# Kernel optimization log

Hardware: AMD Instinct MI355X
Metric: run time of the kernel (lower is better)

The kernel has to match this reference:

```python
import jax, jax.numpy as jnp
import numpy as np

B, N, IN_DIM = 8, 2048, 256
H, D = 8, 64  # num_heads, output_dim (head dim)


def setup_inputs() -> dict:
    key = jax.random.key(0)
    ks = jax.random.split(key, 8)
    s_in = 1.0 / np.sqrt(IN_DIM)
    s_hd = 1.0 / np.sqrt(H * D)
    return {
        "msg": jax.random.normal(ks[0], (B, N, IN_DIM), dtype=jnp.float32),
        "Wq": jax.random.uniform(ks[1], (IN_DIM, H * D), jnp.float32, -s_in, s_in),
        "bq": jax.random.uniform(ks[2], (H * D,), jnp.float32, -s_in, s_in),
        "Wk": jax.random.uniform(ks[3], (IN_DIM, H * D), jnp.float32, -s_in, s_in),
        "bk": jax.random.uniform(ks[4], (H * D,), jnp.float32, -s_in, s_in),
        "Wv": jax.random.uniform(ks[5], (IN_DIM, H * D), jnp.float32, -s_in, s_in),
        "bv": jax.random.uniform(ks[6], (H * D,), jnp.float32, -s_in, s_in),
        "Wo": jax.random.uniform(ks[7], (H * D, D), jnp.float32, -s_hd, s_hd),
    }


def reference(msg, Wq, bq, Wk, bk, Wv, bv, Wo):
    b, n, _ = msg.shape
    # project and split heads: [B, H, N, D]
    q = (msg @ Wq + bq).reshape(b, n, H, D).transpose(0, 2, 1, 3)
    k = (msg @ Wk + bk).reshape(b, n, H, D).transpose(0, 2, 1, 3)
    v = (msg @ Wv + bv).reshape(b, n, H, D).transpose(0, 2, 1, 3)
    # scores in fp32 (original forces float under autocast(enabled=False))
    scores = jnp.einsum("bhnd,bhmd->bhnm", q.astype(jnp.float32), k.astype(jnp.float32)) / jnp.sqrt(jnp.float32(D))
    # exclude-self mask: zero diagonal -> masked with -1e9
    diag = jnp.eye(n, dtype=bool)  # [N, N]
    scores = jnp.where(diag, jnp.float32(-1e9), scores)
    attn = jax.nn.softmax(scores, axis=-1)
    ctx = jnp.einsum("bhnm,bhmd->bhnd", attn, v.astype(jnp.float32))
    ctx = ctx.transpose(0, 2, 1, 3).reshape(b, n, H * D)  # [B, N, H*D]
    return ctx @ Wo  # [B, N, D]
```

## Files before the change

### kernel.cpp

```cpp
#include <hip/hip_runtime.h>

typedef __bf16 bf16;
typedef __bf16 bf16x4 __attribute__((ext_vector_type(4)));
typedef __bf16 bf16x8 __attribute__((ext_vector_type(8)));
typedef float f32x4 __attribute__((ext_vector_type(4)));

#define SCLOG 0.1803368801111244f

constexpr int Bsz = 8, N = 2048, IN = 256, H = 8, D = 64;
constexpr int M = Bsz * N;
constexpr int HD = H * D;
constexpr int QKV = 3 * HD;

__global__ void cvt_msg(const float* __restrict__ in, bf16* __restrict__ out) {
    int i = blockIdx.x * blockDim.x + threadIdx.x;
    float4 v = ((const float4*)in)[i];
    bf16x4 o = { (bf16)v.x, (bf16)v.y, (bf16)v.z, (bf16)v.w };
    ((bf16x4*)out)[i] = o;
}

__global__ __launch_bounds__(256) void pack_w(
    const float* __restrict__ Wq, const float* __restrict__ Wk,
    const float* __restrict__ Wv, const float* __restrict__ bq,
    const float* __restrict__ bk, const float* __restrict__ bv,
    const float* __restrict__ Wo,
    bf16* __restrict__ Wt, float* __restrict__ bias, bf16* __restrict__ Wot) {
    __shared__ float Tt[32][33];
    const int tid = blockIdx.x;
    const int tx = threadIdx.x & 31, ty = threadIdx.x >> 5;
    if (tid < 384) {
        int wsel = tid >> 7, t = tid & 127;
        int k0 = (t >> 4) * 32, cl0 = (t & 15) * 32;
        const float* W = wsel == 0 ? Wq : (wsel == 1 ? Wk : Wv);
#pragma unroll
        for (int i = 0; i < 4; ++i)
            Tt[ty + i * 8][tx] = W[(size_t)(k0 + ty + i * 8) * HD + cl0 + tx];
        __syncthreads();
#pragma unroll
        for (int i = 0; i < 4; ++i)
            Wt[(size_t)(wsel * HD + cl0 + ty + i * 8) * IN + k0 + tx] =
                (bf16)Tt[tx][ty + i * 8];
    } else if (tid < 416) {
        int t = tid - 384;
        int r0 = (t >> 1) * 32, c0 = (t & 1) * 32;
#pragma unroll
        for (int i = 0; i < 4; ++i)
            Tt[ty + i * 8][tx] = Wo[(size_t)(r0 + ty + i * 8) * D + c0 + tx];
        __syncthreads();
#pragma unroll
        for (int i = 0; i < 4; ++i)
            Wot[(size_t)(c0 + ty + i * 8) * HD + r0 + tx] = (bf16)Tt[tx][ty + i * 8];
    } else {
        for (int v = threadIdx.x; v < QKV; v += 256)
            bias[v] = v < HD ? bq[v] : (v < 2 * HD ? bk[v - HD] : bv[v - 2 * HD]);
    }
}

__global__ __launch_bounds__(256) void qkv_gemm(
    const bf16* __restrict__ A, const bf16* __restrict__ Wt,
    const float* __restrict__ bias,
    bf16* __restrict__ Q, bf16* __restrict__ K, bf16* __restrict__ Vt) {
    __shared__ bf16 Tv[128][136];
    const int w = threadIdx.x >> 6, lane = threadIdx.x & 63;
    const int lr = lane & 15, lg = lane >> 4;
    const int mblk = blockIdx.x * 128;
    const int m0 = mblk + w * 32;
    const int c0 = blockIdx.y * 128;

    f32x4 acc[2][8] = {};
    const bf16* ap0 = A + (size_t)(m0 + lr) * IN + lg * 8;
    const bf16* ap1 = A + (size_t)(m0 + 16 + lr) * IN + lg * 8;
    const bf16* bp  = Wt + (size_t)(c0 + lr) * IN + lg * 8;

#pragma unroll
    for (int ks = 0; ks < 8; ++ks) {
        bf16x8 a0 = *(const bf16x8*)(ap0 + ks * 32);
        bf16x8 a1 = *(const bf16x8*)(ap1 + ks * 32);
#pragma unroll
        for (int nt = 0; nt < 8; ++nt) {
            bf16x8 bf = *(const bf16x8*)(bp + (size_t)nt * 16 * IN + ks * 32);
            acc[0][nt] = __builtin_amdgcn_mfma_f32_16x16x32_bf16(a0, bf, acc[0][nt], 0, 0, 0);
            acc[1][nt] = __builtin_amdgcn_mfma_f32_16x16x32_bf16(a1, bf, acc[1][nt], 0, 0, 0);
        }
    }

    if (c0 < 2 * HD) {
        bf16* dst = (c0 < HD) ? Q : K;
#pragma unroll
        for (int mt = 0; mt < 2; ++mt) {
            int rowb = m0 + mt * 16 + lg * 4;
#pragma unroll
            for (int nt = 0; nt < 8; ++nt) {
                int cc = (c0 + nt * 16 + lr) & (HD - 1);
                float bv = bias[c0 + nt * 16 + lr];
                int h = cc >> 6, d = cc & 63;
#pragma unroll
                for (int r = 0; r < 4; ++r) {
                    int row = rowb + r;
                    int b = row >> 11, n = row & (N - 1);
                    dst[(((size_t)(b * H + h) * N) + n) * D + d] =
                        (bf16)(acc[mt][nt][r] + bv);
                }
            }
        }
    } else {
#pragma unroll
        for (int mt = 0; mt < 2; ++mt) {
            int mb = w * 32 + mt * 16 + lg * 4;
#pragma unroll
            for (int nt = 0; nt < 8; ++nt) {
                int cl = nt * 16 + lr;
                float bv = bias[c0 + cl];
                bf16x4 pk = { (bf16)(acc[mt][nt][0] + bv), (bf16)(acc[mt][nt][1] + bv),
                              (bf16)(acc[mt][nt][2] + bv), (bf16)(acc[mt][nt][3] + bv) };
                *(bf16x4*)&Tv[cl][mb] = pk;
            }
        }
        __syncthreads();
        const int cc0 = c0 - 2 * HD;
        const int b = mblk >> 11;
        const int nb = mblk & (N - 1);
        const int j = threadIdx.x & 15;
#pragma unroll
        for (int pass = 0; pass < 8; ++pass) {
            int cl = pass * 16 + (threadIdx.x >> 4);
            int cc = cc0 + cl, h = cc >> 6, d = cc & 63;
            bf16x8 vv = *(const bf16x8*)&Tv[cl][j * 8];
            *(bf16x8*)(Vt + ((size_t)(b * H + h) * D + d) * N + nb + j * 8) = vv;
        }
    }
}

__device__ __forceinline__ void stage_tile(const bf16* __restrict__ srcRowBase,
                                           size_t rowStride, bf16* ldsBase,
                                           int w, int lane) {
    int r8 = lane >> 3;
    int cb = ((lane & 7) ^ r8) << 4;
    const bf16* g = srcRowBase + (size_t)(w * 8 + r8) * rowStride + (cb >> 1);
    bf16* l = ldsBase + w * 8 * 64;
    __builtin_amdgcn_global_load_lds(
        (const __attribute__((address_space(1))) char*)g,
        (__attribute__((address_space(3))) char*)l, 16, 0, 0);
}

__global__ __launch_bounds__(512, 4) void attn_kernel(
    const bf16* __restrict__ Qg, const bf16* __restrict__ Kg,
    const bf16* __restrict__ Vtg, bf16* __restrict__ ctx) {
    __shared__ bf16 Kb[2][64][64];
    __shared__ bf16 Vb[2][64][64];
    __shared__ bf16 P[8][32][64];
    const int w = threadIdx.x >> 6, lane = threadIdx.x & 63;
    const int lr = lane & 15, lg = lane >> 4;
    const int bh = blockIdx.x;
    const int q0 = blockIdx.y * 256 + w * 32;

    const bf16* Qp = Qg + (size_t)bh * N * D;
    const bf16* Kp = Kg + (size_t)bh * N * D;
    const bf16* Vp = Vtg + (size_t)bh * D * N;

    bf16x8 qf[2][2];
#pragma unroll
    for (int qt = 0; qt < 2; ++qt)
#pragma unroll
        for (int kd = 0; kd < 2; ++kd)
            qf[qt][kd] = *(const bf16x8*)(Qp + (size_t)(q0 + qt * 16 + lr) * D + kd * 32 + lg * 8);

    float mrow[2] = { -1e30f, -1e30f };
    float lrow[2] = { 0.f, 0.f };
    f32x4 cacc[2][4] = {};

    stage_tile(Kp, 64, &Kb[0][0][0], w, lane);
    stage_tile(Vp, N,  &Vb[0][0][0], w, lane);
    __syncthreads();
    int cur = 0;

    const int swz = (lr & 7) << 4;
    char* prow0 = (char*)&P[w][lr][0];

    for (int kt = 0; kt < N / 64; ++kt) {
        const int kk0 = kt * 64;
        if (kt + 1 < N / 64) {
            stage_tile(Kp + (size_t)(kk0 + 64) * 64, 64, &Kb[cur ^ 1][0][0], w, lane);
            stage_tile(Vp + (kk0 + 64),         N,  &Vb[cur ^ 1][0][0], w, lane);
        }
        const char* kbase = (const char*)&Kb[cur][0][0];
        f32x4 s[2][4] = {};
#pragma unroll
        for (int nt = 0; nt < 4; ++nt)
#pragma unroll
            for (int kd = 0; kd < 2; ++kd) {
                bf16x8 kf = *(const bf16x8*)(kbase + (nt * 16 + lr) * 128 + ((kd * 64 + lg * 16) ^ swz));
                s[0][nt] = __builtin_amdgcn_mfma_f32_16x16x32_bf16(kf, qf[0][kd], s[0][nt], 0, 0, 0);
                s[1][nt] = __builtin_amdgcn_mfma_f32_16x16x32_bf16(kf, qf[1][kd], s[1][nt], 0, 0, 0);
            }
        if (kk0 < q0 + 32 && q0 < kk0 + 64) {
#pragma unroll
            for (int qt = 0; qt < 2; ++qt) {
                int q = q0 + qt * 16 + lr;
#pragma unroll
                for (int nt = 0; nt < 4; ++nt)
#pragma unroll
                    for (int r = 0; r < 4; ++r)
                        if (kk0 + nt * 16 + lg * 4 + r == q) s[qt][nt][r] = -3e38f;
            }
        }
        float rm[2];
        bool need = false;
#pragma unroll
        for (int qt = 0; qt < 2; ++qt) {
            float v = s[qt][0][0];
#pragma unroll
            for (int nt = 0; nt < 4; ++nt)
#pragma unroll
                for (int r = 0; r < 4; ++r) v = fmaxf(v, s[qt][nt][r]);
            v = fmaxf(v, __shfl_xor(v, 16));
            v = fmaxf(v, __shfl_xor(v, 32));
            rm[qt] = v;
            need = need || (v > mrow[qt] + 64.f);
        }
        if (__any(need)) {
#pragma unroll
            for (int qt = 0; qt < 2; ++qt) {
                float mn = fmaxf(mrow[qt], rm[qt]);
                float f = exp2f((mrow[qt] - mn) * SCLOG);
                mrow[qt] = mn;
                lrow[qt] *= f;
#pragma unroll
                for (int r = 0; r < 4; ++r) {
                    float fr = __shfl(f, lg * 4 + r);
#pragma unroll
                    for (int dt = 0; dt < 4; ++dt) cacc[qt][dt][r] *= fr;
                }
            }
        }
#pragma unroll
        for (int qt = 0; qt < 2; ++qt) {
            float mc = mrow[qt] * SCLOG;
            float ps = 0.f;
            char* prow = prow0 + qt * 2048;
#pragma unroll
            for (int nt = 0; nt < 4; ++nt) {
                float p0 = exp2f(__builtin_fmaf(s[qt][nt][0], SCLOG, -mc));
                float p1 = exp2f(__builtin_fmaf(s[qt][nt][1], SCLOG, -mc));
                float p2 = exp2f(__builtin_fmaf(s[qt][nt][2], SCLOG, -mc));
                float p3 = exp2f(__builtin_fmaf(s[qt][nt][3], SCLOG, -mc));
                ps += (p0 + p1) + (p2 + p3);
                bf16x4 pk = { (bf16)p0, (bf16)p1, (bf16)p2, (bf16)p3 };
                *(bf16x4*)(prow + ((nt * 32 + lg * 8) ^ swz)) = pk;
            }
            ps += __shfl_xor(ps, 16);
            ps += __shfl_xor(ps, 32);
            lrow[qt] += ps;
        }
        const char* vbase = (const char*)&Vb[cur][0][0];
#pragma unroll
        for (int ks = 0; ks < 2; ++ks) {
            bf16x8 pa[2];
#pragma unroll
            for (int qt = 0; qt < 2; ++qt)
                pa[qt] = *(const bf16x8*)(prow0 + qt * 2048 + ((ks * 64 + lg * 16) ^ swz));
#pragma unroll
            for (int dt = 0; dt < 4; ++dt) {
                bf16x8 vf = *(const bf16x8*)(vbase + (dt * 16 + lr) * 128 + ((ks * 64 + lg * 16) ^ swz));
                cacc[0][dt] = __builtin_amdgcn_mfma_f32_16x16x32_bf16(pa[0], vf, cacc[0][dt], 0, 0, 0);
                cacc[1][dt] = __builtin_amdgcn_mfma_f32_16x16x32_bf16(pa[1], vf, cacc[1][dt], 0, 0, 0);
            }
        }
        __syncthreads();
        cur ^= 1;
    }
    const int b = bh >> 3, h = bh & 7;
#pragma unroll
    for (int qt = 0; qt < 2; ++qt) {
        float ool = 1.0f / lrow[qt];
#pragma unroll
        for (int r = 0; r < 4; ++r) {
            float oolr = __shfl(ool, lg * 4 + r);
            int q = q0 + qt * 16 + lg * 4 + r;
#pragma unroll
            for (int dt = 0; dt < 4; ++dt)
                ctx[((size_t)(b * N + q)) * HD + h * 64 + dt * 16 + lr] =
                    (bf16)(cacc[qt][dt][r] * oolr);
        }
    }
}

__global__ __launch_bounds__(256) void out_gemm(
    const bf16* __restrict__ ctx, const bf16* __restrict__ Wot,
    float* __restrict__ out) {
    const int w = threadIdx.x >> 6, lane = threadIdx.x & 63;
    const int lr = lane & 15, lg = lane >> 4;
    const int m0 = blockIdx.x * 64 + w * 16;
    f32x4 acc[4] = {};
#pragma unroll
    for (int ks = 0; ks < 16; ++ks) {
        bf16x8 af = *(const bf16x8*)(ctx + (size_t)(m0 + lr) * HD + ks * 32 + lg * 8);
#pragma unroll
        for (int nt = 0; nt < 4; ++nt) {
            bf16x8 wf = *(const bf16x8*)(Wot + (size_t)(nt * 16 + lr) * HD + ks * 32 + lg * 8);
            acc[nt] = __builtin_amdgcn_mfma_f32_16x16x32_bf16(af, wf, acc[nt], 0, 0, 0);
        }
    }
#pragma unroll
    for (int nt = 0; nt < 4; ++nt)
#pragma unroll
        for (int r = 0; r < 4; ++r)
            out[(size_t)(m0 + lg * 4 + r) * D + nt * 16 + lr] = acc[nt][r];
}

extern "C" void kernel_launch(void* const* d_in, const int* in_sizes, int n_in,
                              void* d_out, int out_size, void* d_ws, size_t ws_size,
                              hipStream_t stream) {
    (void)in_sizes; (void)n_in; (void)out_size; (void)ws_size;
    const float* msg = (const float*)d_in[0];
    const float* Wq  = (const float*)d_in[1];
    const float* bq  = (const float*)d_in[2];
    const float* Wk  = (const float*)d_in[3];
    const float* bk  = (const float*)d_in[4];
    const float* Wv  = (const float*)d_in[5];
    const float* bv  = (const float*)d_in[6];
    const float* Wo  = (const float*)d_in[7];
    float* out = (float*)d_out;

    char* p = (char*)d_ws;
    bf16*  Abf  = (bf16*)p;  p += (size_t)M * IN * 2;
    bf16*  Wt   = (bf16*)p;  p += (size_t)QKV * IN * 2;
    float* bias = (float*)p; p += (size_t)QKV * 4;
    bf16*  Wot  = (bf16*)p;  p += (size_t)D * HD * 2;
    bf16*  Qb   = (bf16*)p;  p += (size_t)Bsz * H * N * D * 2;
    bf16*  Kb   = (bf16*)p;  p += (size_t)Bsz * H * N * D * 2;
    bf16*  Vtb  = (bf16*)p;  p += (size_t)Bsz * H * D * N * 2;
    bf16*  Ctx  = (bf16*)p;  p += (size_t)M * HD * 2;

    cvt_msg<<<(M * IN / 4) / 256, 256, 0, stream>>>(msg, Abf);
    pack_w<<<417, 256, 0, stream>>>(Wq, Wk, Wv, bq, bk, bv, Wo, Wt, bias, Wot);

    dim3 g1(M / 128, QKV / 128);
    qkv_gemm<<<g1, 256, 0, stream>>>(Abf, Wt, bias, Qb, Kb, Vtb);

    dim3 g2(Bsz * H, N / 256);
    attn_kernel<<<g2, 512, 0, stream>>>(Qb, Kb, Vtb, Ctx);

    out_gemm<<<M / 64, 256, 0, stream>>>(Ctx, Wot, out);
}
```

Baseline: 271.4 us.

## Stage QKV GEMM tiles through swizzled LDS and compute softmax row sums via MFMA

The QKV projection GEMM now double-buffers 128x64 A and W tiles into swizzled shared memory using global_load_lds, instead of each wave reading its operands directly from global memory. This is meant to cut redundant global traffic and overlap loads with MFMA work, at the cost of 64KB of LDS per block. In the attention kernel, the softmax row sums are now accumulated with an extra MFMA against a ones vector, using the bf16-rounded probabilities already in LDS. This replaces the scalar adds and cross-lane shuffles, adds MFMA work, and slightly changes the normalisation numerics.

Measured after the change: 226.5 us. -16.5%, faster.

```diff
diff --git a/kernel.cpp b/kernel.cpp
--- a/kernel.cpp
+++ b/kernel.cpp
@@ -11,6 +11,17 @@
 constexpr int M = Bsz * N;
 constexpr int HD = H * D;
 constexpr int QKV = 3 * HD;
+
+__device__ __forceinline__ void stage8(const bf16* __restrict__ src, size_t stride,
+                                       bf16* ldsBase, int row0, int lane) {
+    int r8 = lane >> 3;
+    int cb = ((lane & 7) ^ r8) << 4;
+    const bf16* g = src + (size_t)(row0 + r8) * stride + (cb >> 1);
+    bf16* l = ldsBase + row0 * 64;
+    __builtin_amdgcn_global_load_lds(
+        (const __attribute__((address_space(1))) char*)g,
+        (__attribute__((address_space(3))) char*)l, 16, 0, 0);
+}
 
 __global__ void cvt_msg(const float* __restrict__ in, bf16* __restrict__ out) {
     int i = blockIdx.x * blockDim.x + threadIdx.x;
@@ -60,28 +71,47 @@
     const bf16* __restrict__ A, const bf16* __restrict__ Wt,
     const float* __restrict__ bias,
     bf16* __restrict__ Q, bf16* __restrict__ K, bf16* __restrict__ Vt) {
-    __shared__ bf16 Tv[128][136];
+    __shared__ __align__(16) char smem[65536];
     const int w = threadIdx.x >> 6, lane = threadIdx.x & 63;
     const int lr = lane & 15, lg = lane >> 4;
     const int mblk = blockIdx.x * 128;
     const int m0 = mblk + w * 32;
     const int c0 = blockIdx.y * 128;
+    const int swz = (lr & 7) << 4;
+
+    auto stage_step = [&](int buf, int kk) {
+        bf16* as_ = (bf16*)(smem + buf * 32768);
+        bf16* bs_ = (bf16*)(smem + buf * 32768 + 16384);
+#pragma unroll
+        for (int j = 0; j < 4; ++j) {
+            stage8(A + (size_t)mblk * IN + kk, IN, as_, w * 32 + j * 8, lane);
+            stage8(Wt + (size_t)c0 * IN + kk, IN, bs_, w * 32 + j * 8, lane);
+        }
+    };
 
     f32x4 acc[2][8] = {};
-    const bf16* ap0 = A + (size_t)(m0 + lr) * IN + lg * 8;
-    const bf16* ap1 = A + (size_t)(m0 + 16 + lr) * IN + lg * 8;
-    const bf16* bp  = Wt + (size_t)(c0 + lr) * IN + lg * 8;
-
-#pragma unroll
-    for (int ks = 0; ks < 8; ++ks) {
-        bf16x8 a0 = *(const bf16x8*)(ap0 + ks * 32);
-        bf16x8 a1 = *(const bf16x8*)(ap1 + ks * 32);
-#pragma unroll
-        for (int nt = 0; nt < 8; ++nt) {
-            bf16x8 bf = *(const bf16x8*)(bp + (size_t)nt * 16 * IN + ks * 32);
-            acc[0][nt] = __builtin_amdgcn_mfma_f32_16x16x32_bf16(a0, bf, acc[0][nt], 0, 0, 0);
-            acc[1][nt] = __builtin_amdgcn_mfma_f32_16x16x32_bf16(a1, bf, acc[1][nt], 0, 0, 0);
-        }
+    stage_step(0, 0);
+    __syncthreads();
+    int cur = 0;
+
+    for (int kstep = 0; kstep < 4; ++kstep) {
+        if (kstep < 3) stage_step(cur ^ 1, (kstep + 1) * 64);
+        const char* abase = smem + cur * 32768;
+        const char* bbase = abase + 16384;
+        const char* arow = abase + (w * 32) * 128;
+#pragma unroll
+        for (int ks = 0; ks < 2; ++ks) {
+            bf16x8 a0 = *(const bf16x8*)(arow + lr * 128 + ((ks * 64 + lg * 16) ^ swz));
+            bf16x8 a1 = *(const bf16x8*)(arow + (16 + lr) * 128 + ((ks * 64 + lg * 16) ^ swz));
+#pragma unroll
+            for (int nt = 0; nt < 8; ++nt) {
+                bf16x8 bf = *(const bf16x8*)(bbase + (nt * 16 + lr) * 128 + ((ks * 64 + lg * 16) ^ swz));
+                acc[0][nt] = __builtin_amdgcn_mfma_f32_16x16x32_bf16(a0, bf, acc[0][nt], 0, 0, 0);
+                acc[1][nt] = __builtin_amdgcn_mfma_f32_16x16x32_bf16(a1, bf, acc[1][nt], 0, 0, 0);
+            }
+        }
+        __syncthreads();
+        cur ^= 1;
     }
 
     if (c0 < 2 * HD) {
@@ -104,6 +134,7 @@
             }
         }
     } else {
+        bf16 (*Tv)[136] = (bf16(*)[136])smem;
 #pragma unroll
         for (int mt = 0; mt < 2; ++mt) {
             int mb = w * 32 + mt * 16 + lg * 4;
@@ -129,18 +160,6 @@
             *(bf16x8*)(Vt + ((size_t)(b * H + h) * D + d) * N + nb + j * 8) = vv;
         }
     }
-}
-
-__device__ __forceinline__ void stage_tile(const bf16* __restrict__ srcRowBase,
-                                           size_t rowStride, bf16* ldsBase,
-                                           int w, int lane) {
-    int r8 = lane >> 3;
-    int cb = ((lane & 7) ^ r8) << 4;
-    const bf16* g = srcRowBase + (size_t)(w * 8 + r8) * rowStride + (cb >> 1);
-    bf16* l = ldsBase + w * 8 * 64;
-    __builtin_amdgcn_global_load_lds(
-        (const __attribute__((address_space(1))) char*)g,
-        (__attribute__((address_space(3))) char*)l, 16, 0, 0);
 }
 
 __global__ __launch_bounds__(512, 4) void attn_kernel(
@@ -165,12 +184,15 @@
         for (int kd = 0; kd < 2; ++kd)
             qf[qt][kd] = *(const bf16x8*)(Qp + (size_t)(q0 + qt * 16 + lr) * D + kd * 32 + lg * 8);
 
+    const bf16 onev = (bf16)1.0f;
+    const bf16x8 ones = { onev, onev, onev, onev, onev, onev, onev, onev };
+
     float mrow[2] = { -1e30f, -1e30f };
-    float lrow[2] = { 0.f, 0.f };
+    float lrow[2][4] = {};
     f32x4 cacc[2][4] = {};
 
-    stage_tile(Kp, 64, &Kb[0][0][0], w, lane);
-    stage_tile(Vp, N,  &Vb[0][0][0], w, lane);
+    stage8(Kp, 64, &Kb[0][0][0], w * 8, lane);
+    stage8(Vp, N,  &Vb[0][0][0], w * 8, lane);
     __syncthreads();
     int cur = 0;
 
@@ -180,8 +202,8 @@
     for (int kt = 0; kt < N / 64; ++kt) {
         const int kk0 = kt * 64;
         if (kt + 1 < N / 64) {
-            stage_tile(Kp + (size_t)(kk0 + 64) * 64, 64, &Kb[cur ^ 1][0][0], w, lane);
-            stage_tile(Vp + (kk0 + 64),         N,  &Vb[cur ^ 1][0][0], w, lane);
+            stage8(Kp + (size_t)(kk0 + 64) * 64, 64, &Kb[cur ^ 1][0][0], w * 8, lane);
+            stage8(Vp + (kk0 + 64),         N,  &Vb[cur ^ 1][0][0], w * 8, lane);
         }
         const char* kbase = (const char*)&Kb[cur][0][0];
         f32x4 s[2][4] = {};
@@ -224,10 +246,10 @@
                 float mn = fmaxf(mrow[qt], rm[qt]);
                 float f = exp2f((mrow[qt] - mn) * SCLOG);
                 mrow[qt] = mn;
-                lrow[qt] *= f;
 #pragma unroll
                 for (int r = 0; r < 4; ++r) {
                     float fr = __shfl(f, lg * 4 + r);
+                    lrow[qt][r] *= fr;
 #pragma unroll
                     for (int dt = 0; dt < 4; ++dt) cacc[qt][dt][r] *= fr;
                 }
@@ -236,7 +258,6 @@
 #pragma unroll
         for (int qt = 0; qt < 2; ++qt) {
             float mc = mrow[qt] * SCLOG;
-            float ps = 0.f;
             char* prow = prow0 + qt * 2048;
 #pragma unroll
             for (int nt = 0; nt < 4; ++nt) {
@@ -244,21 +265,20 @@
                 float p1 = exp2f(__builtin_fmaf(s[qt][nt][1], SCLOG, -mc));
                 float p2 = exp2f(__builtin_fmaf(s[qt][nt][2], SCLOG, -mc));
                 float p3 = exp2f(__builtin_fmaf(s[qt][nt][3], SCLOG, -mc));
-                ps += (p0 + p1) + (p2 + p3);
                 bf16x4 pk = { (bf16)p0, (bf16)p1, (bf16)p2, (bf16)p3 };
                 *(bf16x4*)(prow + ((nt * 32 + lg * 8) ^ swz)) = pk;
             }
-            ps += __shfl_xor(ps, 16);
-            ps += __shfl_xor(ps, 32);
-            lrow[qt] += ps;
         }
         const char* vbase = (const char*)&Vb[cur][0][0];
+        f32x4 sacc[2] = {};
 #pragma unroll
         for (int ks = 0; ks < 2; ++ks) {
             bf16x8 pa[2];
 #pragma unroll
-            for (int qt = 0; qt < 2; ++qt)
+            for (int qt = 0; qt < 2; ++qt) {
                 pa[qt] = *(const bf16x8*)(prow0 + qt * 2048 + ((ks * 64 + lg * 16) ^ swz));
+                sacc[qt] = __builtin_amdgcn_mfma_f32_16x16x32_bf16(pa[qt], ones, sacc[qt], 0, 0, 0);
+            }
 #pragma unroll
             for (int dt = 0; dt < 4; ++dt) {
                 bf16x8 vf = *(const bf16x8*)(vbase + (dt * 16 + lr) * 128 + ((ks * 64 + lg * 16) ^ swz));
@@ -266,16 +286,19 @@
                 cacc[1][dt] = __builtin_amdgcn_mfma_f32_16x16x32_bf16(pa[1], vf, cacc[1][dt], 0, 0, 0);
             }
         }
+#pragma unroll
+        for (int qt = 0; qt < 2; ++qt)
+#pragma unroll
+            for (int r = 0; r < 4; ++r) lrow[qt][r] += sacc[qt][r];
         __syncthreads();
         cur ^= 1;
     }
     const int b = bh >> 3, h = bh & 7;
 #pragma unroll
     for (int qt = 0; qt < 2; ++qt) {
-        float ool = 1.0f / lrow[qt];
 #pragma unroll
         for (int r = 0; r < 4; ++r) {
-            float oolr = __shfl(ool, lg * 4 + r);
+            float oolr = 1.0f / lrow[qt][r];
             int q = q0 + qt * 16 + lg * 4 + r;
 #pragma unroll
             for (int dt = 0; dt < 4; ++dt)
```
